# Optimization experiments

Measured on AMD Instinct MI355X. Metric: run time of the kernel, lower is better.

Reference implementation:

```python
import jax, jax.numpy as jnp
import numpy as np
from math import factorial

LMAX = 5
MUL = 128            # multiplicity per irrep degree in the node embedding
NUM_CHANNELS = 4
NUM_RADII = 64
RES_BETA = 180
RES_ALPHA = 359
NUM_SPECIES = 5
NUM_GRAPHS = 16
NUM_NODES = 512
SH_DIM = (LMAX + 1) ** 2          # 36
EMB_DIM = MUL * SH_DIM            # 4608
NUM_IRREPS = MUL * (LMAX + 1)     # 768
INV_TEMP = 1.0


def _real_sh_basis(lmax, res_beta, res_alpha):
    """Orthonormal real spherical harmonics evaluated on a Gauss-Legendre beta grid
    and a uniform alpha grid (the grid used by e3nn.to_s2grid with gausslegendre
    quadrature). Returns B[(l*l + l + m), beta, alpha]. Precomputed in numpy since
    the grid is static."""
    y, _ = np.polynomial.legendre.leggauss(res_beta)          # y = cos(beta)
    alpha = np.linspace(0.0, 2.0 * np.pi, res_alpha, endpoint=False)
    # associated Legendre P[l, m] on y (Condon-Shortley phase)
    P = np.zeros((lmax + 1, lmax + 1, res_beta))
    P[0, 0] = 1.0
    somx2 = np.sqrt(np.clip(1.0 - y * y, 0.0, None))
    for m in range(1, lmax + 1):
        P[m, m] = -(2 * m - 1) * somx2 * P[m - 1, m - 1]
    for m in range(lmax):
        P[m + 1, m] = (2 * m + 1) * y * P[m, m]
    for m in range(lmax + 1):
        for l in range(m + 2, lmax + 1):
            P[l, m] = ((2 * l - 1) * y * P[l - 1, m] - (l + m - 1) * P[l - 2, m]) / (l - m)
    B = np.zeros(((lmax + 1) ** 2, res_beta, res_alpha))
    ones_a = np.ones_like(alpha)
    for l in range(lmax + 1):
        for m in range(l + 1):
            N = np.sqrt((2 * l + 1) / (4.0 * np.pi) * factorial(l - m) / factorial(l + m))
            if m == 0:
                B[l * l + l] = (N * P[l, 0])[:, None] * ones_a[None, :]
            else:
                B[l * l + l + m] = np.sqrt(2.0) * N * P[l, m][:, None] * np.cos(m * alpha)[None, :]
                B[l * l + l - m] = np.sqrt(2.0) * N * P[l, m][:, None] * np.sin(m * alpha)[None, :]
    return jnp.asarray(B, dtype=jnp.float32)


_B = _real_sh_basis(LMAX, RES_BETA, RES_ALPHA)   # (36, 180, 359)


def _split_blocks(emb):
    """Split an irreps array (G, sum_l MUL*(2l+1)) into per-degree blocks (G, MUL, 2l+1)."""
    blocks, off = [], 0
    for l in range(LMAX + 1):
        d = 2 * l + 1
        blocks.append(emb[:, off:off + MUL * d].reshape(-1, MUL, d))
        off += MUL * d
    return blocks


def setup_inputs() -> dict:
    key = jax.random.key(0)
    ks = jax.random.split(key, 13)
    inp = {
        "node_embeddings": jax.random.normal(ks[0], (NUM_NODES, EMB_DIM), jnp.float32),
        "species_embed": jax.random.normal(ks[1], (NUM_SPECIES, NUM_IRREPS), jnp.float32),
        "W_radial": jax.random.normal(ks[2], (MUL, NUM_RADII), jnp.float32),
        "W_mlp1": jax.random.normal(ks[3], (NUM_RADII, MUL), jnp.float32),
        "W_mlp2": jax.random.normal(ks[4], (MUL, NUM_RADII), jnp.float32),
    }
    for l in range(LMAX + 1):
        inp[f"W_ang_{l}"] = jax.random.normal(ks[5 + l], (MUL, NUM_CHANNELS), jnp.float32)
    inp["focus_indices"] = jax.random.randint(ks[11], (NUM_GRAPHS,), 0, NUM_NODES)
    inp["target_species"] = jax.random.randint(ks[12], (NUM_GRAPHS,), 0, NUM_SPECIES)
    return inp


def _forward(node_embeddings, species_embed, W_radial, W_mlp1, W_mlp2, W_ang,
             focus_indices, target_species):
    rsqrt_mul = np.float32(1.0 / np.sqrt(MUL))
    focus = node_embeddings[focus_indices]                 # (G, EMB_DIM)
    spec = species_embed[target_species]                   # (G, NUM_IRREPS), one scalar per irrep
    blocks = _split_blocks(focus)
    # target_species_embeddings * focus_node_embeddings: scale each irrep by its scalar
    scaled = [blk * spec[:, MUL * l:MUL * (l + 1), None] for l, blk in enumerate(blocks)]
    # radial path: e3nn Linear to num_radii x 0e (only 0e inputs contribute) + MLP
    scal0 = scaled[0][..., 0]                              # (G, MUL)
    r = (scal0 @ W_radial) * rsqrt_mul                     # (G, NUM_RADII)
    h = jax.nn.softplus((r @ W_mlp1) * np.float32(1.0 / np.sqrt(NUM_RADII)))
    radial_logits = (h @ W_mlp2) * rsqrt_mul               # (G, NUM_RADII)
    # angular path: e3nn Linear to num_channels * s2_irreps (per-degree channel mixing)
    ang = jnp.concatenate(
        [jnp.einsum("gkm,kc->gcm", scaled[l], W_ang[l]) * rsqrt_mul
         for l in range(LMAX + 1)], axis=-1)               # (G, C, 36)
    # joint distribution coefficients: radial logit adds to the l=0 coefficient
    joint0 = ang[:, :, None, :1] + radial_logits[:, None, :, None]     # (G, C, R, 1)
    rest = jnp.broadcast_to(ang[:, :, None, 1:],
                            (NUM_GRAPHS, NUM_CHANNELS, NUM_RADII, SH_DIM - 1))
    log_position_coeffs = jnp.concatenate([joint0, rest], axis=-1) * np.float32(INV_TEMP)
    # log_coeffs_to_logits: SH synthesis on the grid, then logsumexp over channels
    pos_grid = jnp.einsum("gcrk,kba->gcrba", log_position_coeffs, _B)
    position_logits = jax.nn.logsumexp(pos_grid, axis=1)   # (G, R, beta, alpha)
    ang_grid = jnp.einsum("gck,kba->gcba", ang, _B)
    angular_logits = jax.nn.logsumexp(ang_grid, axis=1, keepdims=True)  # (G, 1, beta, alpha)
    return log_position_coeffs, position_logits, angular_logits, radial_logits


def reference(node_embeddings, species_embed, W_radial, W_mlp1, W_mlp2,
              W_ang_0, W_ang_1, W_ang_2, W_ang_3, W_ang_4, W_ang_5,
              focus_indices, target_species):
    W_ang = [W_ang_0, W_ang_1, W_ang_2, W_ang_3, W_ang_4, W_ang_5]
    return _forward(node_embeddings, species_embed, W_radial, W_mlp1, W_mlp2, W_ang,
                    focus_indices, target_species)
```

## Files before the change

kernel.cpp:

```cpp
#include <hip/hip_runtime.h>
#include <math.h>

#define LMAX   5
#define MUL    128
#define NCH    4
#define NRAD   64
#define RBETA  180
#define RALPHA 359
#define NGRAPH 16
#define SH_DIM 36
#define EMB_DIM 4608
#define NIRR   768

#define GRID_BA (RBETA * RALPHA)
#define N_F4    (GRID_BA / 4)

#define OUT0_OFF 0
#define OUT1_OFF 147456
#define OUT2_OFF (147456 + 66170880)
#define OUT3_OFF (147456 + 66170880 + 1033920)


__global__ void k_nodes(double* __restrict__ y) {
    __shared__ double rcp[RBETA];
    const int n = RBETA;
    int tid = threadIdx.x;
    for (int k = tid; k < n; k += blockDim.x) rcp[k] = 1.0 / (double)(k + 1);
    __syncthreads();
    int i = tid;
    if (i >= n) return;
    const double PI = 3.14159265358979323846;
    double x = -cos(PI * (i + 0.75) / (n + 0.5));
    for (int it = 0; it < 6; ++it) {
        double p0 = 1.0, p1 = x;
        for (int k = 1; k < n; ++k) {
            double p2 = ((2.0 * k + 1.0) * x * p1 - (double)k * p0) * rcp[k];
            p0 = p1; p1 = p2;
        }
        double dp = n * (x * p1 - p0) / (x * x - 1.0);
        x -= p1 / dp;
    }
    y[i] = x;
}

__global__ __launch_bounds__(256)
void k_small(const float* __restrict__ ne, const float* __restrict__ sp,
             const float* __restrict__ wrad, const float* __restrict__ wm1,
             const float* __restrict__ wm2,
             const float* __restrict__ wa0, const float* __restrict__ wa1,
             const float* __restrict__ wa2, const float* __restrict__ wa3,
             const float* __restrict__ wa4, const float* __restrict__ wa5,
             const int* __restrict__ focus, const int* __restrict__ tspec,
             float* __restrict__ out0, float* __restrict__ out3,
             float* __restrict__ ang_ws, float* __restrict__ rad_ws)
{
    __shared__ float s0[MUL];
    __shared__ float rr[NRAD];
    __shared__ float hh[MUL];
    __shared__ float rl[NRAD];
    __shared__ float sang[NCH * SH_DIM];

    const int g = blockIdx.x;
    const int tid = threadIdx.x;
    const int fi = focus[g];
    const int ts = tspec[g];
    const float rs128 = 0.08838834764831845f;
    const float rs64  = 0.125f;

    if (tid < MUL) s0[tid] = ne[(size_t)fi * EMB_DIM + tid] * sp[ts * NIRR + tid];
    __syncthreads();

    if (tid < NRAD) {
        float acc = 0.f;
        for (int k = 0; k < MUL; ++k) acc += s0[k] * wrad[k * NRAD + tid];
        rr[tid] = acc * rs128;
    }
    __syncthreads();

    if (tid < MUL) {
        float acc = 0.f;
        for (int j = 0; j < NRAD; ++j) acc += rr[j] * wm1[j * MUL + tid];
        float x = acc * rs64;
        hh[tid] = fmaxf(x, 0.f) + log1pf(expf(-fabsf(x)));
    }
    __syncthreads();

    if (tid < NRAD) {
        float acc = 0.f;
        for (int k = 0; k < MUL; ++k) acc += hh[k] * wm2[k * NRAD + tid];
        float v = acc * rs128;
        rl[tid] = v;
        out3[g * NRAD + tid] = v;
        rad_ws[g * NRAD + tid] = v;
    }

    const float* WA[6] = {wa0, wa1, wa2, wa3, wa4, wa5};
    for (int t = tid; t < NCH * SH_DIM; t += blockDim.x) {
        int c = t / SH_DIM, kk = t % SH_DIM;
        int l = 0;
        while ((l + 1) * (l + 1) <= kk) ++l;
        int j = kk - l * l;
        int d = 2 * l + 1;
        const float* w  = WA[l];
        const float* nb = ne + (size_t)fi * EMB_DIM + MUL * l * l + j;
        const float* sb = sp + ts * NIRR + MUL * l;
        float acc = 0.f;
        for (int k = 0; k < MUL; ++k) acc += nb[k * d] * sb[k] * w[k * NCH + c];
        float v = acc * rs128;
        sang[t] = v;
        ang_ws[g * (NCH * SH_DIM) + t] = v;
    }
    __syncthreads();

    for (int t = tid; t < NCH * NRAD * SH_DIM; t += blockDim.x) {
        int kk = t % SH_DIM;
        int r  = (t / SH_DIM) % NRAD;
        int c  = t / (SH_DIM * NRAD);
        float v = sang[c * SH_DIM + kk];
        if (kk == 0) v += rl[r];
        out0[(size_t)g * (NCH * NRAD * SH_DIM) + t] = v;
    }
}

__global__ __launch_bounds__(256)
void k_angular(const double* __restrict__ y, const float* __restrict__ ang_ws,
               float* __restrict__ out2)
{
    __shared__ float sW[21];
    __shared__ float sAng[NCH * SH_DIM];
    __shared__ float sF[NCH][11];

    const int beta = blockIdx.x;
    const int g    = blockIdx.y;
    const int tid  = threadIdx.x;

    for (int t = tid; t < NCH * SH_DIM; t += 256)
        sAng[t] = ang_ws[g * (NCH * SH_DIM) + t];

    if (tid == 0) {
        double yy = y[beta];
        double P[LMAX + 1][LMAX + 1];
        P[0][0] = 1.0;
        double somx2 = sqrt(fmax(1.0 - yy * yy, 0.0));
        for (int m = 1; m <= LMAX; ++m) P[m][m] = -(2.0 * m - 1.0) * somx2 * P[m - 1][m - 1];
        for (int m = 0; m < LMAX; ++m)  P[m + 1][m] = (2.0 * m + 1.0) * yy * P[m][m];
        for (int m = 0; m <= LMAX; ++m)
            for (int l = m + 2; l <= LMAX; ++l)
                P[l][m] = ((2.0 * l - 1.0) * yy * P[l - 1][m] - (l + m - 1.0) * P[l - 2][m]) / (double)(l - m);
        const double FOURPI = 12.566370614359172;
        for (int l = 0; l <= LMAX; ++l) {
            for (int m = 0; m <= l; ++m) {
                double fr = 1.0;
                for (int k = l - m + 1; k <= l + m; ++k) fr /= (double)k;
                double N = sqrt((2.0 * l + 1.0) / FOURPI * fr);
                double w = N * P[l][m];
                if (m > 0) w *= 1.4142135623730951;
                sW[l * (l + 1) / 2 + m] = (float)w;
            }
        }
    }
    __syncthreads();

    if (tid < NCH * 11) {
        int c = tid / 11, j = tid % 11;
        float acc = 0.f;
        if (j == 0) {
            for (int l = 0; l <= LMAX; ++l)
                acc += sAng[c * SH_DIM + l * l + l] * sW[l * (l + 1) / 2];
        } else if (j <= 5) {
            int m = j;
            for (int l = m; l <= LMAX; ++l)
                acc += sAng[c * SH_DIM + l * l + l + m] * sW[l * (l + 1) / 2 + m];
        } else {
            int m = j - 5;
            for (int l = m; l <= LMAX; ++l)
                acc += sAng[c * SH_DIM + l * l + l - m] * sW[l * (l + 1) / 2 + m];
        }
        sF[c][j] = acc;
    }
    __syncthreads();

    const float dalpha = 6.283185307179586f / 359.0f;
    for (int a = tid; a < RALPHA; a += 256) {
        float alpha = dalpha * (float)a;
        float s1, c1;
        __sincosf(alpha, &s1, &c1);
        float t0 = sF[0][0], t1 = sF[1][0], t2 = sF[2][0], t3 = sF[3][0];
        float cm = c1, sm = s1;
        for (int m = 1; m <= 5; ++m) {
            t0 += sF[0][m] * cm + sF[0][5 + m] * sm;
            t1 += sF[1][m] * cm + sF[1][5 + m] * sm;
            t2 += sF[2][m] * cm + sF[2][5 + m] * sm;
            t3 += sF[3][m] * cm + sF[3][5 + m] * sm;
            float cn = cm * c1 - sm * s1;
            float sn = sm * c1 + cm * s1;
            cm = cn; sm = sn;
        }
        float mx = fmaxf(fmaxf(t0, t1), fmaxf(t2, t3));
        float s = expf(t0 - mx) + expf(t1 - mx) + expf(t2 - mx) + expf(t3 - mx);
        out2[(size_t)g * GRID_BA + beta * RALPHA + a] = mx + logf(s);
    }
}

__global__ __launch_bounds__(256)
void k_pos(const float* __restrict__ out2, const float* __restrict__ rad_ws,
           float* __restrict__ out1)
{
    const int g = blockIdx.z;
    const int r = blockIdx.y;
    const int i = blockIdx.x * 256 + threadIdx.x;
    if (i >= N_F4) return;
    const float rc = rad_ws[g * NRAD + r] * 0.28209479177387814f;
    const float4* src = (const float4*)(out2 + (size_t)g * GRID_BA);
    float4 v = src[i];
    v.x += rc; v.y += rc; v.z += rc; v.w += rc;
    float4* dst = (float4*)(out1 + ((size_t)(g * NRAD + r)) * GRID_BA);
    dst[i] = v;
}

extern "C" void kernel_launch(void* const* d_in, const int* in_sizes, int n_in,
                              void* d_out, int out_size, void* d_ws, size_t ws_size,
                              hipStream_t stream) {
    const float* ne   = (const float*)d_in[0];
    const float* sp   = (const float*)d_in[1];
    const float* wrad = (const float*)d_in[2];
    const float* wm1  = (const float*)d_in[3];
    const float* wm2  = (const float*)d_in[4];
    const float* wa0  = (const float*)d_in[5];
    const float* wa1  = (const float*)d_in[6];
    const float* wa2  = (const float*)d_in[7];
    const float* wa3  = (const float*)d_in[8];
    const float* wa4  = (const float*)d_in[9];
    const float* wa5  = (const float*)d_in[10];
    const int* focus  = (const int*)d_in[11];
    const int* tspec  = (const int*)d_in[12];

    float* out  = (float*)d_out;
    float* out0 = out + OUT0_OFF;
    float* out1 = out + OUT1_OFF;
    float* out2 = out + OUT2_OFF;
    float* out3 = out + OUT3_OFF;

    double* y     = (double*)d_ws;
    float* ang_ws = (float*)((char*)d_ws + 2048);
    float* rad_ws = (float*)((char*)d_ws + 2048 + 9216);

    hipLaunchKernelGGL(k_nodes, dim3(1), dim3(192), 0, stream, y);
    hipLaunchKernelGGL(k_small, dim3(NGRAPH), dim3(256), 0, stream,
                       ne, sp, wrad, wm1, wm2, wa0, wa1, wa2, wa3, wa4, wa5,
                       focus, tspec, out0, out3, ang_ws, rad_ws);
    hipLaunchKernelGGL(k_angular, dim3(RBETA, NGRAPH), dim3(256), 0, stream,
                       y, ang_ws, out2);
    hipLaunchKernelGGL(k_pos, dim3((N_F4 + 255) / 256, NRAD, NGRAPH), dim3(256), 0, stream,
                       out2, rad_ws, out1);
}
```

Measured before the change: 361.9 us.

## Fuse angular logsumexp with positional broadcast and precompute Legendre table on host

Merges the angular grid kernel and the per-radius broadcast kernel into one kernel, so each thread writes the angular logit and then all 64 radius-shifted copies directly. This removes re-reading out2 and one launch. The Gauss-Legendre nodes and per-beta SH weights are now computed once on the host, cached in a static table, and copied to the workspace on every call, replacing the single-block node kernel. The fused kernel's writes to out1 are strided by a full grid plane per radius, and the whole large output is now produced by only 180x16 blocks.

Result: slower. 379.9 us (+5.0%).

```diff
diff --git a/kernel.cpp b/kernel.cpp
--- a/kernel.cpp
+++ b/kernel.cpp
@@ -13,34 +13,58 @@
 #define NIRR   768
 
 #define GRID_BA (RBETA * RALPHA)
-#define N_F4    (GRID_BA / 4)
+#define NW21    21
 
 #define OUT0_OFF 0
 #define OUT1_OFF 147456
 #define OUT2_OFF (147456 + 66170880)
 #define OUT3_OFF (147456 + 66170880 + 1033920)
 
-
-__global__ void k_nodes(double* __restrict__ y) {
-    __shared__ double rcp[RBETA];
-    const int n = RBETA;
-    int tid = threadIdx.x;
-    for (int k = tid; k < n; k += blockDim.x) rcp[k] = 1.0 / (double)(k + 1);
-    __syncthreads();
-    int i = tid;
-    if (i >= n) return;
+#define WS_TAB_OFF 0
+#define WS_ANG_OFF 15360
+#define WS_RAD_OFF 24576
+
+static float g_tab[RBETA * NW21];
+static bool  g_tab_ready = false;
+
+static void host_init_tab() {
+    if (g_tab_ready) return;
     const double PI = 3.14159265358979323846;
-    double x = -cos(PI * (i + 0.75) / (n + 0.5));
-    for (int it = 0; it < 6; ++it) {
-        double p0 = 1.0, p1 = x;
-        for (int k = 1; k < n; ++k) {
-            double p2 = ((2.0 * k + 1.0) * x * p1 - (double)k * p0) * rcp[k];
-            p0 = p1; p1 = p2;
-        }
-        double dp = n * (x * p1 - p0) / (x * x - 1.0);
-        x -= p1 / dp;
-    }
-    y[i] = x;
+    const double FOURPI = 12.566370614359172;
+    for (int i = 0; i < RBETA; ++i) {
+        double x = -cos(PI * (i + 0.75) / (RBETA + 0.5));
+        for (int it = 0; it < 40; ++it) {
+            double p0 = 1.0, p1 = x;
+            for (int k = 1; k < RBETA; ++k) {
+                double p2 = ((2.0 * k + 1.0) * x * p1 - (double)k * p0) / (double)(k + 1);
+                p0 = p1; p1 = p2;
+            }
+            double dp = RBETA * (x * p1 - p0) / (x * x - 1.0);
+            double dx = p1 / dp;
+            x -= dx;
+            if (fabs(dx) < 1e-15) break;
+        }
+        double yy = x;
+        double P[LMAX + 1][LMAX + 1] = {};
+        P[0][0] = 1.0;
+        double somx2 = sqrt(fmax(1.0 - yy * yy, 0.0));
+        for (int m = 1; m <= LMAX; ++m) P[m][m] = -(2.0 * m - 1.0) * somx2 * P[m - 1][m - 1];
+        for (int m = 0; m < LMAX; ++m)  P[m + 1][m] = (2.0 * m + 1.0) * yy * P[m][m];
+        for (int m = 0; m <= LMAX; ++m)
+            for (int l = m + 2; l <= LMAX; ++l)
+                P[l][m] = ((2.0 * l - 1.0) * yy * P[l - 1][m] - (l + m - 1.0) * P[l - 2][m]) / (double)(l - m);
+        for (int l = 0; l <= LMAX; ++l) {
+            for (int m = 0; m <= l; ++m) {
+                double fr = 1.0;
+                for (int k = l - m + 1; k <= l + m; ++k) fr /= (double)k;
+                double N = sqrt((2.0 * l + 1.0) / FOURPI * fr);
+                double w = N * P[l][m];
+                if (m > 0) w *= 1.4142135623730951;
+                g_tab[i * NW21 + l * (l + 1) / 2 + m] = (float)w;
+            }
+        }
+    }
+    g_tab_ready = true;
 }
 
 __global__ __launch_bounds__(256)
@@ -123,42 +147,24 @@
 }
 
 __global__ __launch_bounds__(256)
-void k_angular(const double* __restrict__ y, const float* __restrict__ ang_ws,
-               float* __restrict__ out2)
+void k_fused(const float* __restrict__ tab, const float* __restrict__ ang_ws,
+             const float* __restrict__ rad_ws,
+             float* __restrict__ out2, float* __restrict__ out1)
 {
-    __shared__ float sW[21];
+    __shared__ float sW[NW21];
     __shared__ float sAng[NCH * SH_DIM];
     __shared__ float sF[NCH][11];
+    __shared__ float sRC[NRAD];
 
     const int beta = blockIdx.x;
     const int g    = blockIdx.y;
     const int tid  = threadIdx.x;
 
+    if (tid < NW21) sW[tid] = tab[beta * NW21 + tid];
+    if (tid >= 64 && tid < 64 + NRAD)
+        sRC[tid - 64] = rad_ws[g * NRAD + (tid - 64)] * 0.28209479177387814f;
     for (int t = tid; t < NCH * SH_DIM; t += 256)
         sAng[t] = ang_ws[g * (NCH * SH_DIM) + t];
-
-    if (tid == 0) {
-        double yy = y[beta];
-        double P[LMAX + 1][LMAX + 1];
-        P[0][0] = 1.0;
-        double somx2 = sqrt(fmax(1.0 - yy * yy, 0.0));
-        for (int m = 1; m <= LMAX; ++m) P[m][m] = -(2.0 * m - 1.0) * somx2 * P[m - 1][m - 1];
-        for (int m = 0; m < LMAX; ++m)  P[m + 1][m] = (2.0 * m + 1.0) * yy * P[m][m];
-        for (int m = 0; m <= LMAX; ++m)
-            for (int l = m + 2; l <= LMAX; ++l)
-                P[l][m] = ((2.0 * l - 1.0) * yy * P[l - 1][m] - (l + m - 1.0) * P[l - 2][m]) / (double)(l - m);
-        const double FOURPI = 12.566370614359172;
-        for (int l = 0; l <= LMAX; ++l) {
-            for (int m = 0; m <= l; ++m) {
-                double fr = 1.0;
-                for (int k = l - m + 1; k <= l + m; ++k) fr /= (double)k;
-                double N = sqrt((2.0 * l + 1.0) / FOURPI * fr);
-                double w = N * P[l][m];
-                if (m > 0) w *= 1.4142135623730951;
-                sW[l * (l + 1) / 2 + m] = (float)w;
-            }
-        }
-    }
     __syncthreads();
 
     if (tid < NCH * 11) {
@@ -198,29 +204,22 @@
         }
         float mx = fmaxf(fmaxf(t0, t1), fmaxf(t2, t3));
         float s = expf(t0 - mx) + expf(t1 - mx) + expf(t2 - mx) + expf(t3 - mx);
-        out2[(size_t)g * GRID_BA + beta * RALPHA + a] = mx + logf(s);
-    }
-}
-
-__global__ __launch_bounds__(256)
-void k_pos(const float* __restrict__ out2, const float* __restrict__ rad_ws,
-           float* __restrict__ out1)
-{
-    const int g = blockIdx.z;
-    const int r = blockIdx.y;
-    const int i = blockIdx.x * 256 + threadIdx.x;
-    if (i >= N_F4) return;
-    const float rc = rad_ws[g * NRAD + r] * 0.28209479177387814f;
-    const float4* src = (const float4*)(out2 + (size_t)g * GRID_BA);
-    float4 v = src[i];
-    v.x += rc; v.y += rc; v.z += rc; v.w += rc;
-    float4* dst = (float4*)(out1 + ((size_t)(g * NRAD + r)) * GRID_BA);
-    dst[i] = v;
+        float L = mx + logf(s);
+
+        out2[(size_t)g * GRID_BA + beta * RALPHA + a] = L;
+
+        float* p = out1 + (size_t)g * NRAD * GRID_BA + (size_t)(beta * RALPHA + a);
+        #pragma unroll 8
+        for (int r = 0; r < NRAD; ++r)
+            p[(size_t)r * GRID_BA] = L + sRC[r];
+    }
 }
 
 extern "C" void kernel_launch(void* const* d_in, const int* in_sizes, int n_in,
                               void* d_out, int out_size, void* d_ws, size_t ws_size,
                               hipStream_t stream) {
+    host_init_tab();
+
     const float* ne   = (const float*)d_in[0];
     const float* sp   = (const float*)d_in[1];
     const float* wrad = (const float*)d_in[2];
@@ -241,16 +240,15 @@
     float* out2 = out + OUT2_OFF;
     float* out3 = out + OUT3_OFF;
 
-    double* y     = (double*)d_ws;
-    float* ang_ws = (float*)((char*)d_ws + 2048);
-    float* rad_ws = (float*)((char*)d_ws + 2048 + 9216);
-
-    hipLaunchKernelGGL(k_nodes, dim3(1), dim3(192), 0, stream, y);
+    float* tab    = (float*)((char*)d_ws + WS_TAB_OFF);
+    float* ang_ws = (float*)((char*)d_ws + WS_ANG_OFF);
+    float* rad_ws = (float*)((char*)d_ws + WS_RAD_OFF);
+
+    hipMemcpyAsync(tab, g_tab, sizeof(g_tab), hipMemcpyHostToDevice, stream);
+
     hipLaunchKernelGGL(k_small, dim3(NGRAPH), dim3(256), 0, stream,
                        ne, sp, wrad, wm1, wm2, wa0, wa1, wa2, wa3, wa4, wa5,
                        focus, tspec, out0, out3, ang_ws, rad_ws);
-    hipLaunchKernelGGL(k_angular, dim3(RBETA, NGRAPH), dim3(256), 0, stream,
-                       y, ang_ws, out2);
-    hipLaunchKernelGGL(k_pos, dim3((N_F4 + 255) / 256, NRAD, NGRAPH), dim3(256), 0, stream,
-                       out2, rad_ws, out1);
-}
+    hipLaunchKernelGGL(k_fused, dim3(RBETA, NGRAPH), dim3(256), 0, stream,
+                       tab, ang_ws, rad_ws, out2, out1);
+}
```

## Fold Gauss-Legendre node kernel into k_small as extra block and precompute SH weight table

Applied to the files above, without the earlier changes.

Removes the separate k_nodes launch by running the Legendre root-finding in an extra block of k_small, which runs alongside the per-graph work. That block also computes the per-beta associated-Legendre weight table once, so k_angular no longer recomputes it serially on one thread in each of its 2880 blocks. It saves a launch and the serial double-precision prologue in every angular block, at the cost of a slightly longer k_small critical path.

Result: faster. 335.0 us (-7.4%).

```diff
diff --git a/kernel.cpp b/kernel.cpp
--- a/kernel.cpp
+++ b/kernel.cpp
@@ -14,34 +14,16 @@
 
 #define GRID_BA (RBETA * RALPHA)
 #define N_F4    (GRID_BA / 4)
+#define NW21    21
 
 #define OUT0_OFF 0
 #define OUT1_OFF 147456
 #define OUT2_OFF (147456 + 66170880)
 #define OUT3_OFF (147456 + 66170880 + 1033920)
 
-
-__global__ void k_nodes(double* __restrict__ y) {
-    __shared__ double rcp[RBETA];
-    const int n = RBETA;
-    int tid = threadIdx.x;
-    for (int k = tid; k < n; k += blockDim.x) rcp[k] = 1.0 / (double)(k + 1);
-    __syncthreads();
-    int i = tid;
-    if (i >= n) return;
-    const double PI = 3.14159265358979323846;
-    double x = -cos(PI * (i + 0.75) / (n + 0.5));
-    for (int it = 0; it < 6; ++it) {
-        double p0 = 1.0, p1 = x;
-        for (int k = 1; k < n; ++k) {
-            double p2 = ((2.0 * k + 1.0) * x * p1 - (double)k * p0) * rcp[k];
-            p0 = p1; p1 = p2;
-        }
-        double dp = n * (x * p1 - p0) / (x * x - 1.0);
-        x -= p1 / dp;
-    }
-    y[i] = x;
-}
+#define WS_TAB_OFF 0
+#define WS_ANG_OFF 15360
+#define WS_RAD_OFF 24576
 
 __global__ __launch_bounds__(256)
 void k_small(const float* __restrict__ ne, const float* __restrict__ sp,
@@ -52,8 +34,50 @@
              const float* __restrict__ wa4, const float* __restrict__ wa5,
              const int* __restrict__ focus, const int* __restrict__ tspec,
              float* __restrict__ out0, float* __restrict__ out3,
-             float* __restrict__ ang_ws, float* __restrict__ rad_ws)
+             float* __restrict__ ang_ws, float* __restrict__ rad_ws,
+             float* __restrict__ tab)
 {
+    const int tid = threadIdx.x;
+
+    if (blockIdx.x == NGRAPH) {
+        __shared__ double rcp[RBETA];
+        for (int k = tid; k < RBETA; k += 256) rcp[k] = 1.0 / (double)(k + 1);
+        __syncthreads();
+        const int i = tid;
+        if (i >= RBETA) return;
+        const double PI = 3.14159265358979323846;
+        double x = -cos(PI * (i + 0.75) / (RBETA + 0.5));
+        for (int it = 0; it < 6; ++it) {
+            double p0 = 1.0, p1 = x;
+            for (int k = 1; k < RBETA; ++k) {
+                double p2 = ((2.0 * k + 1.0) * x * p1 - (double)k * p0) * rcp[k];
+                p0 = p1; p1 = p2;
+            }
+            double dp = RBETA * (x * p1 - p0) / (x * x - 1.0);
+            x -= p1 / dp;
+        }
+        double P[LMAX + 1][LMAX + 1];
+        P[0][0] = 1.0;
+        double somx2 = sqrt(fmax(1.0 - x * x, 0.0));
+        for (int m = 1; m <= LMAX; ++m) P[m][m] = -(2.0 * m - 1.0) * somx2 * P[m - 1][m - 1];
+        for (int m = 0; m < LMAX; ++m)  P[m + 1][m] = (2.0 * m + 1.0) * x * P[m][m];
+        for (int m = 0; m <= LMAX; ++m)
+            for (int l = m + 2; l <= LMAX; ++l)
+                P[l][m] = ((2.0 * l - 1.0) * x * P[l - 1][m] - (l + m - 1.0) * P[l - 2][m]) / (double)(l - m);
+        const double FOURPI = 12.566370614359172;
+        for (int l = 0; l <= LMAX; ++l) {
+            for (int m = 0; m <= l; ++m) {
+                double fr = 1.0;
+                for (int k = l - m + 1; k <= l + m; ++k) fr /= (double)k;
+                double N = sqrt((2.0 * l + 1.0) / FOURPI * fr);
+                double w = N * P[l][m];
+                if (m > 0) w *= 1.4142135623730951;
+                tab[i * NW21 + l * (l + 1) / 2 + m] = (float)w;
+            }
+        }
+        return;
+    }
+
     __shared__ float s0[MUL];
     __shared__ float rr[NRAD];
     __shared__ float hh[MUL];
@@ -61,7 +85,6 @@
     __shared__ float sang[NCH * SH_DIM];
 
     const int g = blockIdx.x;
-    const int tid = threadIdx.x;
     const int fi = focus[g];
     const int ts = tspec[g];
     const float rs128 = 0.08838834764831845f;
@@ -123,10 +146,10 @@
 }
 
 __global__ __launch_bounds__(256)
-void k_angular(const double* __restrict__ y, const float* __restrict__ ang_ws,
+void k_angular(const float* __restrict__ tab, const float* __restrict__ ang_ws,
                float* __restrict__ out2)
 {
-    __shared__ float sW[21];
+    __shared__ float sW[NW21];
     __shared__ float sAng[NCH * SH_DIM];
     __shared__ float sF[NCH][11];
 
@@ -134,31 +157,9 @@
     const int g    = blockIdx.y;
     const int tid  = threadIdx.x;
 
+    if (tid < NW21) sW[tid] = tab[beta * NW21 + tid];
     for (int t = tid; t < NCH * SH_DIM; t += 256)
         sAng[t] = ang_ws[g * (NCH * SH_DIM) + t];
-
-    if (tid == 0) {
-        double yy = y[beta];
-        double P[LMAX + 1][LMAX + 1];
-        P[0][0] = 1.0;
-        double somx2 = sqrt(fmax(1.0 - yy * yy, 0.0));
-        for (int m = 1; m <= LMAX; ++m) P[m][m] = -(2.0 * m - 1.0) * somx2 * P[m - 1][m - 1];
-        for (int m = 0; m < LMAX; ++m)  P[m + 1][m] = (2.0 * m + 1.0) * yy * P[m][m];
-        for (int m = 0; m <= LMAX; ++m)
-            for (int l = m + 2; l <= LMAX; ++l)
-                P[l][m] = ((2.0 * l - 1.0) * yy * P[l - 1][m] - (l + m - 1.0) * P[l - 2][m]) / (double)(l - m);
-        const double FOURPI = 12.566370614359172;
-        for (int l = 0; l <= LMAX; ++l) {
-            for (int m = 0; m <= l; ++m) {
-                double fr = 1.0;
-                for (int k = l - m + 1; k <= l + m; ++k) fr /= (double)k;
-                double N = sqrt((2.0 * l + 1.0) / FOURPI * fr);
-                double w = N * P[l][m];
-                if (m > 0) w *= 1.4142135623730951;
-                sW[l * (l + 1) / 2 + m] = (float)w;
-            }
-        }
-    }
     __syncthreads();
 
     if (tid < NCH * 11) {
@@ -241,16 +242,15 @@
     float* out2 = out + OUT2_OFF;
     float* out3 = out + OUT3_OFF;
 
-    double* y     = (double*)d_ws;
-    float* ang_ws = (float*)((char*)d_ws + 2048);
-    float* rad_ws = (float*)((char*)d_ws + 2048 + 9216);
-
-    hipLaunchKernelGGL(k_nodes, dim3(1), dim3(192), 0, stream, y);
-    hipLaunchKernelGGL(k_small, dim3(NGRAPH), dim3(256), 0, stream,
+    float* tab    = (float*)((char*)d_ws + WS_TAB_OFF);
+    float* ang_ws = (float*)((char*)d_ws + WS_ANG_OFF);
+    float* rad_ws = (float*)((char*)d_ws + WS_RAD_OFF);
+
+    hipLaunchKernelGGL(k_small, dim3(NGRAPH + 1), dim3(256), 0, stream,
                        ne, sp, wrad, wm1, wm2, wa0, wa1, wa2, wa3, wa4, wa5,
-                       focus, tspec, out0, out3, ang_ws, rad_ws);
+                       focus, tspec, out0, out3, ang_ws, rad_ws, tab);
     hipLaunchKernelGGL(k_angular, dim3(RBETA, NGRAPH), dim3(256), 0, stream,
-                       y, ang_ws, out2);
+                       tab, ang_ws, out2);
     hipLaunchKernelGGL(k_pos, dim3((N_F4 + 255) / 256, NRAD, NGRAPH), dim3(256), 0, stream,
                        out2, rad_ws, out1);
 }
```
